# Optimization experiments

Measured on AMD Instinct MI355X. Metric: run time of the kernel, lower is better.

## Reference

```python
import jax, jax.numpy as jnp
from jax import lax
import numpy as np

K = 3          # kernel_size (must be 3 for shape consistency with the 3x3 sigma conv)
STRIDE = 2
C_IN = 128
EPS = 1e-5     # FrozenBatchNorm2d eps


def setup_inputs() -> dict:
    key = jax.random.key(0)
    k1, k2, k3, k4, k5, k6 = jax.random.split(key, 6)
    x = jax.random.normal(k1, (8, C_IN, 112, 112), dtype=jnp.float32)
    # conv: in_channels -> k*k, 3x3, no bias (kaiming init ~ normal scaled)
    fan_out = K * K * 3 * 3
    conv_w = jax.random.normal(k2, (K * K, C_IN, 3, 3), dtype=jnp.float32) * np.sqrt(2.0 / fan_out)
    bn_w = jax.random.normal(k3, (K * K,), dtype=jnp.float32) * 0.1 + 1.0
    bn_b = jax.random.normal(k4, (K * K,), dtype=jnp.float32) * 0.1
    bn_mean = jax.random.normal(k5, (K * K,), dtype=jnp.float32) * 0.1
    bn_var = jax.random.uniform(k6, (K * K,), dtype=jnp.float32, minval=0.5, maxval=1.5)
    return {"x": x, "conv_w": conv_w, "bn_w": bn_w, "bn_b": bn_b,
            "bn_mean": bn_mean, "bn_var": bn_var}


def _pasa(x, conv_w, bn_w, bn_b, bn_mean, bn_var):
    n, c, h, w = x.shape
    pad = K // 2
    # reflection pad
    xp = jnp.pad(x, ((0, 0), (0, 0), (pad, pad), (pad, pad)), mode="reflect")
    # 3x3 conv, stride 1, VALID on padded input -> same h, w
    sigma = lax.conv_general_dilated(xp, conv_w, (1, 1), "VALID",
                                     dimension_numbers=("NCHW", "OIHW", "NCHW"))
    # frozen BN: affine with fixed running stats
    scale = bn_w / jnp.sqrt(bn_var + EPS)
    shift = bn_b - bn_mean * scale
    sigma = sigma * scale[None, :, None, None] + shift[None, :, None, None]
    sigma = jnp.clip(sigma, 0.0001)                       # clamp min only
    sigma = sigma.reshape(n, 1, K * K, h * w)
    sigma = sigma / jnp.sum(sigma, axis=2, keepdims=True)  # normalize over k*k
    # unfold: k*k shifted views of the padded input (channel-outer, kernel row-major)
    patches = jnp.stack([xp[:, :, i:i + h, j:j + w]
                         for i in range(K) for j in range(K)], axis=2)  # (n,c,9,h,w)
    out = jnp.sum(patches.reshape(n, c, K * K, h * w) * sigma, axis=2).reshape(n, c, h, w)
    return out[:, :, ::STRIDE, ::STRIDE]


def reference(x, conv_w, bn_w, bn_b, bn_mean, bn_var):
    return _pasa(x, conv_w, bn_w, bn_b, bn_mean, bn_var)
```

## Files before the change

kernel.cpp:

```cpp
#include <hip/hip_runtime.h>

#define NB   8
#define C    128
#define H    112
#define W    112
#define HW   (H * W)
#define HO   56
#define WO   56
#define KK   9
#define WAVES 16
#define PPW  4
#define WPW  (PPW * 81)

typedef float v2f __attribute__((ext_vector_type(2)));

__device__ inline v2f pkfma(v2f a, v2f b, v2f c) {
    return __builtin_elementwise_fma(a, b, c);
}

__global__ __launch_bounds__(1024, 8)
void pasa_main(const float* __restrict__ x,
               const float* __restrict__ cw,
               const float* __restrict__ bw,
               const float* __restrict__ bb,
               const float* __restrict__ bm,
               const float* __restrict__ bv,
               float* __restrict__ out) {
    __shared__ v2f   wlds[WAVES][WPW];
    __shared__ float part[WAVES * KK * 64];
    __shared__ float sig[KK * 57];

    const int bid  = blockIdx.x;
    const int n    = bid & 7;
    const int ho   = bid >> 3;
    const int tid  = threadIdx.x;
    const int lane = tid & 63;
    const int wv   = __builtin_amdgcn_readfirstlane(tid >> 6);
    const int wo   = lane < WO ? lane : (WO - 1);

    const int r0 = (ho == 0) ? 1 : (2 * ho - 1);
    const int r1 = 2 * ho;
    const int r2 = 2 * ho + 1;

    const float* xn = x + (size_t)n * C * HW + 2 * wo;
    const int p0 = wv * PPW;

    for (int i = lane; i < WPW; i += 64) {
        const int p   = i / 81;
        const int rem = i % 81;
        const int kh  = rem / 27;
        const int rr  = rem % 27;
        const int k   = rr / 3;
        const int kw  = rr % 3;
        const float scale = bw[k] * rsqrtf(bv[k] + 1e-5f);
        const int ca = 2 * (p0 + p);
        v2f w2;
        w2.x = cw[((k * C + ca)     * 3 + kh) * 3 + kw] * scale;
        w2.y = cw[((k * C + ca + 1) * 3 + kh) * 3 + kw] * scale;
        wlds[wv][i] = w2;
    }

    v2f acc[KK];
#pragma unroll
    for (int k = 0; k < KK; ++k) acc[k] = (v2f){0.0f, 0.0f};

#pragma unroll 2
    for (int p = 0; p < PPW; ++p) {
        const float* xa = xn + (size_t)(2 * (p0 + p)) * HW;
        const float* xb = xa + HW;
        v2f rowa[3], rowb[3];
        rowa[0] = *(const v2f*)(xa + r0 * W);
        rowa[1] = *(const v2f*)(xa + r1 * W);
        rowa[2] = *(const v2f*)(xa + r2 * W);
        rowb[0] = *(const v2f*)(xb + r0 * W);
        rowb[1] = *(const v2f*)(xb + r1 * W);
        rowb[2] = *(const v2f*)(xb + r2 * W);
#pragma unroll
        for (int kh = 0; kh < 3; ++kh) {
            v2f t1 = { rowa[kh].x, rowb[kh].x };
            v2f t2 = { rowa[kh].y, rowb[kh].y };
            v2f t0;
            t0.x = __shfl_up(t2.x, 1);
            t0.y = __shfl_up(t2.y, 1);
            const v2f* wr = &wlds[wv][p * 81 + kh * 27];
#pragma unroll
            for (int k = 0; k < KK; ++k)
                acc[k] = pkfma(t2, wr[3 * k + 2],
                          pkfma(t1, wr[3 * k + 1],
                          pkfma(t0, wr[3 * k + 0], acc[k])));
        }
    }

#pragma unroll
    for (int k = 0; k < KK; ++k)
        part[(wv * KK + k) * 64 + lane] = acc[k].x + acc[k].y;
    __syncthreads();

    if (tid < KK * WO) {
        const int k  = tid / WO;
        const int w_ = tid % WO;
        float s = 0.0f;
#pragma unroll
        for (int w2 = 0; w2 < WAVES; ++w2) s += part[(w2 * KK + k) * 64 + w_];
        const float scale = bw[k] * rsqrtf(bv[k] + 1e-5f);
        s += bb[k] - bm[k] * scale;
        s = fmaxf(s, 1e-4f);
        sig[k * 57 + w_] = s;
    }
    __syncthreads();

    float sg[KK];
    float tot = 0.0f;
#pragma unroll
    for (int k = 0; k < KK; ++k) { sg[k] = sig[k * 57 + wo]; tot += sg[k]; }
    const float inv = 1.0f / tot;
#pragma unroll
    for (int k = 0; k < KK; ++k) sg[k] *= inv;

    float* on = out + ((size_t)n * C) * (HO * WO) + (size_t)ho * WO + lane;
#pragma unroll 2
    for (int p = 0; p < PPW; ++p) {
        const float* xa = xn + (size_t)(2 * (p0 + p)) * HW;
        const float* xb = xa + HW;
        v2f o = (v2f){0.0f, 0.0f};
#pragma unroll
        for (int kh = 0; kh < 3; ++kh) {
            const int rr = (kh == 0) ? r0 : (kh == 1) ? r1 : r2;
            v2f a = *(const v2f*)(xa + rr * W);
            v2f b = *(const v2f*)(xb + rr * W);
            v2f t1 = { a.x, b.x };
            v2f t2 = { a.y, b.y };
            v2f t0;
            t0.x = __shfl_up(t2.x, 1);
            t0.y = __shfl_up(t2.y, 1);
            v2f s0 = { sg[kh * 3 + 0], sg[kh * 3 + 0] };
            v2f s1 = { sg[kh * 3 + 1], sg[kh * 3 + 1] };
            v2f s2 = { sg[kh * 3 + 2], sg[kh * 3 + 2] };
            o = pkfma(t2, s2, pkfma(t1, s1, pkfma(t0, s0, o)));
        }
        if (lane < WO) {
            const int ci = 2 * (p0 + p);
            __builtin_nontemporal_store(o.x, on + (size_t)ci * (HO * WO));
            __builtin_nontemporal_store(o.y, on + (size_t)(ci + 1) * (HO * WO));
        }
    }
}

extern "C" void kernel_launch(void* const* d_in, const int* in_sizes, int n_in,
                              void* d_out, int out_size, void* d_ws, size_t ws_size,
                              hipStream_t stream) {
    const float* x   = (const float*)d_in[0];
    const float* cw  = (const float*)d_in[1];
    const float* bw  = (const float*)d_in[2];
    const float* bb  = (const float*)d_in[3];
    const float* bm  = (const float*)d_in[4];
    const float* bv  = (const float*)d_in[5];
    float* out = (float*)d_out;
    (void)d_ws; (void)ws_size;

    pasa_main<<<NB * HO, 1024, 0, stream>>>(x, cw, bw, bb, bm, bv, out);
}
```

Measured before the change: 121.6 us.

## Replace LDS-staged packed-FMA conv with scalar per-channel loop reading weights directly

Removes the per-wave LDS staging of BN-scaled weight pairs and the packed two-channel v2f FMA scheme. Each wave now processes 8 channels one at a time with scalar FMAs, reading conv weights straight from global memory as uniform loads, and applies the BN scale after the cross-wave reduction. This avoids the weight-staging prologue and LDS reads but gives up packed-math throughput, and it also lowers the launch-bounds occupancy hint.

```diff
diff --git a/kernel.cpp b/kernel.cpp
--- a/kernel.cpp
+++ b/kernel.cpp
@@ -9,16 +9,11 @@
 #define WO   56
 #define KK   9
 #define WAVES 16
-#define PPW  4
-#define WPW  (PPW * 81)
+#define CPW  8
 
 typedef float v2f __attribute__((ext_vector_type(2)));
 
-__device__ inline v2f pkfma(v2f a, v2f b, v2f c) {
-    return __builtin_elementwise_fma(a, b, c);
-}
-
-__global__ __launch_bounds__(1024, 8)
+__global__ __launch_bounds__(1024, 4)
 void pasa_main(const float* __restrict__ x,
                const float* __restrict__ cw,
                const float* __restrict__ bw,
@@ -26,7 +21,6 @@
                const float* __restrict__ bm,
                const float* __restrict__ bv,
                float* __restrict__ out) {
-    __shared__ v2f   wlds[WAVES][WPW];
     __shared__ float part[WAVES * KK * 64];
     __shared__ float sig[KK * 57];
 
@@ -43,57 +37,41 @@
     const int r2 = 2 * ho + 1;
 
     const float* xn = x + (size_t)n * C * HW + 2 * wo;
-    const int p0 = wv * PPW;
+    const int c0 = wv * CPW;
 
-    for (int i = lane; i < WPW; i += 64) {
-        const int p   = i / 81;
-        const int rem = i % 81;
-        const int kh  = rem / 27;
-        const int rr  = rem % 27;
-        const int k   = rr / 3;
-        const int kw  = rr % 3;
-        const float scale = bw[k] * rsqrtf(bv[k] + 1e-5f);
-        const int ca = 2 * (p0 + p);
-        v2f w2;
-        w2.x = cw[((k * C + ca)     * 3 + kh) * 3 + kw] * scale;
-        w2.y = cw[((k * C + ca + 1) * 3 + kh) * 3 + kw] * scale;
-        wlds[wv][i] = w2;
-    }
-
-    v2f acc[KK];
+    float acc[KK];
 #pragma unroll
-    for (int k = 0; k < KK; ++k) acc[k] = (v2f){0.0f, 0.0f};
+    for (int k = 0; k < KK; ++k) acc[k] = 0.0f;
 
 #pragma unroll 2
-    for (int p = 0; p < PPW; ++p) {
-        const float* xa = xn + (size_t)(2 * (p0 + p)) * HW;
-        const float* xb = xa + HW;
-        v2f rowa[3], rowb[3];
-        rowa[0] = *(const v2f*)(xa + r0 * W);
-        rowa[1] = *(const v2f*)(xa + r1 * W);
-        rowa[2] = *(const v2f*)(xa + r2 * W);
-        rowb[0] = *(const v2f*)(xb + r0 * W);
-        rowb[1] = *(const v2f*)(xb + r1 * W);
-        rowb[2] = *(const v2f*)(xb + r2 * W);
+    for (int c = 0; c < CPW; ++c) {
+        const float* xc = xn + (size_t)(c0 + c) * HW;
+        v2f ra = *(const v2f*)(xc + r0 * W);
+        v2f rb = *(const v2f*)(xc + r1 * W);
+        v2f rc = *(const v2f*)(xc + r2 * W);
+        float t1[3] = { ra.x, rb.x, rc.x };
+        float t2[3] = { ra.y, rb.y, rc.y };
+        float t0[3];
 #pragma unroll
-        for (int kh = 0; kh < 3; ++kh) {
-            v2f t1 = { rowa[kh].x, rowb[kh].x };
-            v2f t2 = { rowa[kh].y, rowb[kh].y };
-            v2f t0;
-            t0.x = __shfl_up(t2.x, 1);
-            t0.y = __shfl_up(t2.y, 1);
-            const v2f* wr = &wlds[wv][p * 81 + kh * 27];
+        for (int kh = 0; kh < 3; ++kh) t0[kh] = __shfl_up(t2[kh], 1);
+
+        const float* wc = cw + (size_t)(c0 + c) * 9;
 #pragma unroll
-            for (int k = 0; k < KK; ++k)
-                acc[k] = pkfma(t2, wr[3 * k + 2],
-                          pkfma(t1, wr[3 * k + 1],
-                          pkfma(t0, wr[3 * k + 0], acc[k])));
+        for (int k = 0; k < KK; ++k) {
+            const float* w = wc + (size_t)k * (C * 9);
+            float a = acc[k];
+#pragma unroll
+            for (int kh = 0; kh < 3; ++kh)
+                a = fmaf(t0[kh], w[kh * 3 + 0],
+                    fmaf(t1[kh], w[kh * 3 + 1],
+                    fmaf(t2[kh], w[kh * 3 + 2], a)));
+            acc[k] = a;
         }
     }
 
 #pragma unroll
     for (int k = 0; k < KK; ++k)
-        part[(wv * KK + k) * 64 + lane] = acc[k].x + acc[k].y;
+        part[(wv * KK + k) * 64 + lane] = acc[k];
     __syncthreads();
 
     if (tid < KK * WO) {
@@ -103,7 +81,8 @@
 #pragma unroll
         for (int w2 = 0; w2 < WAVES; ++w2) s += part[(w2 * KK + k) * 64 + w_];
         const float scale = bw[k] * rsqrtf(bv[k] + 1e-5f);
-        s += bb[k] - bm[k] * scale;
+        const float shift = bb[k] - bm[k] * scale;
+        s = fmaf(scale, s, shift);
         s = fmaxf(s, 1e-4f);
         sig[k * 57 + w_] = s;
     }
@@ -119,29 +98,23 @@
 
     float* on = out + ((size_t)n * C) * (HO * WO) + (size_t)ho * WO + lane;
 #pragma unroll 2
-    for (int p = 0; p < PPW; ++p) {
-        const float* xa = xn + (size_t)(2 * (p0 + p)) * HW;
-        const float* xb = xa + HW;
-        v2f o = (v2f){0.0f, 0.0f};
+    for (int c = 0; c < CPW; ++c) {
+        const float* xc = xn + (size_t)(c0 + c) * HW;
+        v2f ra = *(const v2f*)(xc + r0 * W);
+        v2f rb = *(const v2f*)(xc + r1 * W);
+        v2f rc = *(const v2f*)(xc + r2 * W);
+        float t1[3] = { ra.x, rb.x, rc.x };
+        float t2[3] = { ra.y, rb.y, rc.y };
+        float o = 0.0f;
 #pragma unroll
         for (int kh = 0; kh < 3; ++kh) {
-            const int rr = (kh == 0) ? r0 : (kh == 1) ? r1 : r2;
-            v2f a = *(const v2f*)(xa + rr * W);
-            v2f b = *(const v2f*)(xb + rr * W);
-            v2f t1 = { a.x, b.x };
-            v2f t2 = { a.y, b.y };
-            v2f t0;
-            t0.x = __shfl_up(t2.x, 1);
-            t0.y = __shfl_up(t2.y, 1);
-            v2f s0 = { sg[kh * 3 + 0], sg[kh * 3 + 0] };
-            v2f s1 = { sg[kh * 3 + 1], sg[kh * 3 + 1] };
-            v2f s2 = { sg[kh * 3 + 2], sg[kh * 3 + 2] };
-            o = pkfma(t2, s2, pkfma(t1, s1, pkfma(t0, s0, o)));
+            float t0 = __shfl_up(t2[kh], 1);
+            o = fmaf(t0,     sg[kh * 3 + 0],
+                fmaf(t1[kh], sg[kh * 3 + 1],
+                fmaf(t2[kh], sg[kh * 3 + 2], o)));
         }
         if (lane < WO) {
-            const int ci = 2 * (p0 + p);
-            __builtin_nontemporal_store(o.x, on + (size_t)ci * (HO * WO));
-            __builtin_nontemporal_store(o.y, on + (size_t)(ci + 1) * (HO * WO));
+            __builtin_nontemporal_store(o, on + (size_t)(c0 + c) * (HO * WO));
         }
     }
 }
```

New measurement: 112.5 us. -7.5%, faster.
